# Optimization experiments

Measured on AMD Instinct MI355X. Metric: run time of the kernel, lower is better.

## Reference

```python
import jax, jax.numpy as jnp
import numpy as np

N_NODES = 100000
N_EDGES = 800000
F_IN, N_HID, N_CLS = 256, 128, 40


def setup_inputs() -> dict:
    key = jax.random.key(0)
    ks = jax.random.split(key, 6)
    features = jax.random.normal(ks[0], (N_NODES, F_IN), dtype=jnp.float32)
    src = jax.random.randint(ks[1], (N_EDGES,), 0, N_NODES, dtype=jnp.int64)
    dst = jax.random.randint(ks[2], (N_EDGES,), 0, N_NODES, dtype=jnp.int64)
    W1 = jax.random.normal(ks[3], (F_IN, N_HID), dtype=jnp.float32) / np.sqrt(F_IN)
    b1 = jnp.zeros((N_HID,), dtype=jnp.float32)
    W2 = jax.random.normal(ks[4], (N_HID, N_CLS), dtype=jnp.float32) / np.sqrt(N_HID)
    b2 = jnp.zeros((N_CLS,), dtype=jnp.float32)
    return {"features": features, "src": src, "dst": dst,
            "W1": W1, "b1": b1, "W2": W2, "b2": b2}


def reference(features, src, dst, W1, b1, W2, b2):
    # DGL GraphConv with norm='both': h = D_dst^{-1/2} A (D_src^{-1/2} x) W + b
    # Eval mode: dropout(p=0.85) is identity.
    N = features.shape[0]
    ones = jnp.ones(src.shape[0], dtype=features.dtype)
    out_deg = jax.ops.segment_sum(ones, src, num_segments=N)
    in_deg = jax.ops.segment_sum(ones, dst, num_segments=N)
    norm_src = jnp.where(out_deg > 0, out_deg ** -0.5, 0.0)[:, None]  # [N,1]
    norm_dst = jnp.where(in_deg > 0, in_deg ** -0.5, 0.0)[:, None]

    def gconv(x, W, b):
        # project first (in_feats >= out_feats here) to shrink SpMM width
        h = (x * norm_src) @ W                                # [N, out]
        agg = jax.ops.segment_sum(h[src], dst, num_segments=N)  # sparse aggregate
        return agg * norm_dst + b

    x = jax.nn.relu(gconv(features, W1, b1))
    return gconv(x, W2, b2)
```

## Files before the change

### kernel.cpp

```cpp
#include <hip/hip_runtime.h>
#include <hip/hip_bf16.h>
#include <math.h>


#define F_IN  256
#define F_HID 128
#define F_CLS 40

#define RSZ 8192
#define NSL 32

typedef __bf16 bf16_t;
typedef bf16_t bf16x8 __attribute__((ext_vector_type(8)));
typedef float floatx4 __attribute__((ext_vector_type(4)));

static __device__ __forceinline__ unsigned short f2b(float f) {
    __hip_bfloat16 h = __float2bfloat16(f);
    return __builtin_bit_cast(unsigned short, h);
}
static __device__ __forceinline__ float b2f(unsigned short u) {
    return __uint_as_float((unsigned)u << 16);
}
static __device__ __forceinline__ unsigned short f2h(float f) {
    return __builtin_bit_cast(unsigned short, (_Float16)f);
}
static __device__ __forceinline__ float h2f(unsigned short u) {
    return (float)__builtin_bit_cast(_Float16, u);
}

__global__ __launch_bounds__(256) void hist_kernel(
    const int* __restrict__ src, const int* __restrict__ dst,
    unsigned* __restrict__ partial_s, unsigned* __restrict__ partial_d, int E)
{
    __shared__ unsigned h[RSZ];
    const int t = threadIdx.x;
    const int r  = blockIdx.x / NSL;
    const int sl = blockIdx.x % NSL;
    const int lo = r * RSZ;
    const int* __restrict__ keys = blockIdx.y ? dst : src;
    unsigned* __restrict__ part = blockIdx.y ? partial_d : partial_s;

    for (int i = t; i < RSZ; i += 256) h[i] = 0;
    __syncthreads();

    const int slice = (E + NSL - 1) / NSL;
    const int e0 = sl * slice;
    const int e1 = min(E, e0 + slice);

    int e = e0 + t;
    for (; e + 7 * 256 < e1; e += 8 * 256) {
        int k[8];
        #pragma unroll
        for (int i = 0; i < 8; ++i) k[i] = keys[e + i * 256];
        #pragma unroll
        for (int i = 0; i < 8; ++i) {
            unsigned kk = (unsigned)(k[i] - lo);
            if (kk < RSZ) atomicAdd(&h[kk], 1u);
        }
    }
    for (; e < e1; e += 256) {
        unsigned kk = (unsigned)(keys[e] - lo);
        if (kk < RSZ) atomicAdd(&h[kk], 1u);
    }
    __syncthreads();

    unsigned* dst_p = part + (size_t)blockIdx.x * RSZ;
    for (int i = t; i < RSZ; i += 256) dst_p[i] = h[i];
}

__global__ __launch_bounds__(256) void degnorm_kernel(
    const unsigned* __restrict__ partial_s, const unsigned* __restrict__ partial_d,
    int* __restrict__ cnt_dst, float* __restrict__ norm_src,
    float* __restrict__ norm_dst, int N)
{
    int i = blockIdx.x * 256 + threadIdx.x;
    if (i >= N) return;
    int r = i / RSZ;
    int off = i & (RSZ - 1);
    const unsigned* ps = partial_s + (size_t)r * NSL * RSZ + off;
    const unsigned* pd = partial_d + (size_t)r * NSL * RSZ + off;
    unsigned ss = 0, sd = 0;
    #pragma unroll
    for (int sl = 0; sl < NSL; ++sl) {
        ss += ps[(size_t)sl * RSZ];
        sd += pd[(size_t)sl * RSZ];
    }
    cnt_dst[i] = (int)sd;
    norm_src[i] = ss ? 1.0f / sqrtf((float)ss) : 0.0f;
    norm_dst[i] = sd ? 1.0f / sqrtf((float)sd) : 0.0f;
}

__global__ __launch_bounds__(256) void scan1_kernel(const int* __restrict__ cnt,
                                                    int* __restrict__ row_off,
                                                    int* __restrict__ blk_sums, int N) {
    __shared__ int s[256];
    const int t = threadIdx.x;
    const int base = blockIdx.x * 1024 + t * 4;
    int v0 = (base + 0 < N) ? cnt[base + 0] : 0;
    int v1 = (base + 1 < N) ? cnt[base + 1] : 0;
    int v2 = (base + 2 < N) ? cnt[base + 2] : 0;
    int v3 = (base + 3 < N) ? cnt[base + 3] : 0;
    int local = v0 + v1 + v2 + v3;
    s[t] = local;
    __syncthreads();
    for (int off = 1; off < 256; off <<= 1) {
        int x = (t >= off) ? s[t - off] : 0;
        __syncthreads();
        s[t] += x;
        __syncthreads();
    }
    int excl = s[t] - local;
    if (t == 255) blk_sums[blockIdx.x] = s[t];
    if (base + 0 < N) row_off[base + 0] = excl;
    if (base + 1 < N) row_off[base + 1] = excl + v0;
    if (base + 2 < N) row_off[base + 2] = excl + v0 + v1;
    if (base + 3 < N) row_off[base + 3] = excl + v0 + v1 + v2;
}

__global__ __launch_bounds__(256) void scan2_kernel(int* __restrict__ blk_sums, int B) {
    __shared__ int s[256];
    const int t = threadIdx.x;
    int local = (t < B) ? blk_sums[t] : 0;
    s[t] = local;
    __syncthreads();
    for (int off = 1; off < 256; off <<= 1) {
        int x = (t >= off) ? s[t - off] : 0;
        __syncthreads();
        s[t] += x;
        __syncthreads();
    }
    if (t < B) blk_sums[t] = s[t] - local;
}

__global__ __launch_bounds__(256) void scan3_kernel(int* __restrict__ row_off,
                                                    const int* __restrict__ blk_sums,
                                                    int N, int E) {
    const int t = threadIdx.x;
    const int base = blockIdx.x * 1024 + t * 4;
    const int add = blk_sums[blockIdx.x];
    #pragma unroll
    for (int i = 0; i < 4; ++i) {
        int idx = base + i;
        if (idx < N) row_off[idx] += add;
    }
    if (blockIdx.x == 0 && t == 0) row_off[N] = E;
}

__global__ __launch_bounds__(256) void slicepref_kernel(
    unsigned* __restrict__ partial_d, const int* __restrict__ row_off,
    int N, int NRtot)
{
    int idx = blockIdx.x * 256 + threadIdx.x;
    if (idx >= NRtot) return;
    int r = idx / RSZ;
    int i = idx & (RSZ - 1);
    unsigned run = (idx < N) ? (unsigned)row_off[idx] : 0u;
    unsigned* p = partial_d + (size_t)r * NSL * RSZ + i;
    #pragma unroll
    for (int sl = 0; sl < NSL; ++sl) {
        unsigned c = p[(size_t)sl * RSZ];
        p[(size_t)sl * RSZ] = run;
        run += c;
    }
}

__global__ __launch_bounds__(256) void scatter2_kernel(
    const int* __restrict__ src, const int* __restrict__ dst,
    const unsigned* __restrict__ pref, int* __restrict__ csr_src, int E)
{
    __shared__ unsigned cur[RSZ];
    const int t = threadIdx.x;
    const int r  = blockIdx.x / NSL;
    const int sl = blockIdx.x % NSL;
    const int lo = r * RSZ;
    const unsigned* p = pref + (size_t)blockIdx.x * RSZ;

    for (int i = t; i < RSZ; i += 256) cur[i] = p[i];
    __syncthreads();

    const int slice = (E + NSL - 1) / NSL;
    const int e0 = sl * slice;
    const int e1 = min(E, e0 + slice);

    int e = e0 + t;
    for (; e + 7 * 256 < e1; e += 8 * 256) {
        int d[8], s[8];
        #pragma unroll
        for (int i = 0; i < 8; ++i) { d[i] = dst[e + i * 256]; s[i] = src[e + i * 256]; }
        #pragma unroll
        for (int i = 0; i < 8; ++i) {
            unsigned k = (unsigned)(d[i] - lo);
            if (k < RSZ) {
                unsigned pos = atomicAdd(&cur[k], 1u);
                csr_src[pos] = s[i];
            }
        }
    }
    for (; e < e1; e += 256) {
        unsigned k = (unsigned)(dst[e] - lo);
        if (k < RSZ) {
            unsigned pos = atomicAdd(&cur[k], 1u);
            csr_src[pos] = src[e];
        }
    }
}

__global__ __launch_bounds__(256) void pack_w1t_kernel(const float* __restrict__ W1,
                                                       __hip_bfloat16* __restrict__ W1t) {
    int idx = blockIdx.x * 256 + threadIdx.x;
    int n = idx >> 8;
    int k = idx & 255;
    W1t[idx] = __float2bfloat16(W1[(size_t)k * F_HID + n]);
}

__global__ __launch_bounds__(512, 4) void gemm1_mfma_kernel(
    const float* __restrict__ X, const __hip_bfloat16* __restrict__ W1t,
    const float* __restrict__ norm_src, __hip_bfloat16* __restrict__ h1b, int N)
{
    __shared__ __hip_bfloat16 Bs[128 * 256];
    const int t = threadIdx.x;
    const int node0 = blockIdx.x * 128;
    const int lane = t & 63;
    const int w = t >> 6;
    const int l15 = lane & 15;
    const int quad = lane >> 4;

    const int arow = node0 + w * 16 + l15;
    const bool valid = arow < N;
    const int arow_c = valid ? arow : (N - 1);
    const float ns = valid ? norm_src[arow] : 0.0f;

    const float* xp = X + (size_t)arow_c * F_IN + quad * 8;

    float4 araw[4];
    araw[0] = *(const float4*)(xp + 0);
    araw[1] = *(const float4*)(xp + 4);
    araw[2] = *(const float4*)(xp + 32);
    araw[3] = *(const float4*)(xp + 36);

    #pragma unroll
    for (int i = 0; i < 8; ++i) {
        int idx = i * 512 + t;
        int row = idx >> 5;
        int ch  = idx & 31;
        uint4 v = *(const uint4*)(W1t + (size_t)row * F_IN + ch * 8);
        int d = row * 256 + ((ch * 8) ^ ((row & 7) << 3));
        *(uint4*)(Bs + d) = v;
    }
    __syncthreads();

    const int swz = (l15 & 7) << 3;
    const int bbase0 = l15 * 256 + ((quad * 8) ^ swz);
    const int bbase1 = l15 * 256 + ((32 + quad * 8) ^ swz);

    floatx4 acc[8] = {};

    #pragma unroll
    for (int c = 0; c < 4; ++c) {
        bf16x8 ab0, ab1;
        {
            union { bf16x8 v; unsigned short u[8]; } cv;
            cv.u[0] = f2b(araw[0].x * ns); cv.u[1] = f2b(araw[0].y * ns);
            cv.u[2] = f2b(araw[0].z * ns); cv.u[3] = f2b(araw[0].w * ns);
            cv.u[4] = f2b(araw[1].x * ns); cv.u[5] = f2b(araw[1].y * ns);
            cv.u[6] = f2b(araw[1].z * ns); cv.u[7] = f2b(araw[1].w * ns);
            ab0 = cv.v;
            cv.u[0] = f2b(araw[2].x * ns); cv.u[1] = f2b(araw[2].y * ns);
            cv.u[2] = f2b(araw[2].z * ns); cv.u[3] = f2b(araw[2].w * ns);
            cv.u[4] = f2b(araw[3].x * ns); cv.u[5] = f2b(araw[3].y * ns);
            cv.u[6] = f2b(araw[3].z * ns); cv.u[7] = f2b(araw[3].w * ns);
            ab1 = cv.v;
        }
        if (c < 3) {
            araw[0] = *(const float4*)(xp + (c + 1) * 64 + 0);
            araw[1] = *(const float4*)(xp + (c + 1) * 64 + 4);
            araw[2] = *(const float4*)(xp + (c + 1) * 64 + 32);
            araw[3] = *(const float4*)(xp + (c + 1) * 64 + 36);
        }
        #pragma unroll
        for (int nt = 0; nt < 8; ++nt) {
            bf16x8 b = *(const bf16x8*)(Bs + bbase0 + nt * 16 * 256 + c * 64);
            acc[nt] = __builtin_amdgcn_mfma_f32_16x16x32_bf16(ab0, b, acc[nt], 0, 0, 0);
        }
        #pragma unroll
        for (int nt = 0; nt < 8; ++nt) {
            bf16x8 b = *(const bf16x8*)(Bs + bbase1 + nt * 16 * 256 + c * 64);
            acc[nt] = __builtin_amdgcn_mfma_f32_16x16x32_bf16(ab1, b, acc[nt], 0, 0, 0);
        }
    }

    #pragma unroll
    for (int nt = 0; nt < 8; ++nt) {
        #pragma unroll
        for (int r = 0; r < 4; ++r) {
            int node = node0 + w * 16 + quad * 4 + r;
            if (node < N)
                h1b[(size_t)node * F_HID + nt * 16 + l15] = __float2bfloat16(acc[nt][r]);
        }
    }
}

__global__ __launch_bounds__(256) void spmm1_csr_kernel(
    const __hip_bfloat16* __restrict__ h1b, const int* __restrict__ row_off,
    const int* __restrict__ csr_src, const float* __restrict__ norm_src,
    const float* __restrict__ norm_dst, const float* __restrict__ b1,
    unsigned short* __restrict__ h1act, int N)
{
    const int t = threadIdx.x;
    const int node = blockIdx.x * 8 + (t >> 5);
    if (node >= N) return;
    const int c = (t & 31) << 2;
    const int start = row_off[node];
    const int end = row_off[node + 1];
    float4 acc = make_float4(0.f, 0.f, 0.f, 0.f);
    int j = start;
    for (; j + 8 <= end; j += 8) {
        int s[8];
        #pragma unroll
        for (int i = 0; i < 8; ++i) s[i] = csr_src[j + i];
        ushort4 u[8];
        #pragma unroll
        for (int i = 0; i < 8; ++i)
            u[i] = *(const ushort4*)(h1b + (size_t)s[i] * F_HID + c);
        #pragma unroll
        for (int i = 0; i < 8; ++i) {
            acc.x += b2f(u[i].x);
            acc.y += b2f(u[i].y);
            acc.z += b2f(u[i].z);
            acc.w += b2f(u[i].w);
        }
    }
    for (; j + 2 <= end; j += 2) {
        int s0 = csr_src[j + 0];
        int s1 = csr_src[j + 1];
        ushort4 u0 = *(const ushort4*)(h1b + (size_t)s0 * F_HID + c);
        ushort4 u1 = *(const ushort4*)(h1b + (size_t)s1 * F_HID + c);
        acc.x += b2f(u0.x) + b2f(u1.x);
        acc.y += b2f(u0.y) + b2f(u1.y);
        acc.z += b2f(u0.z) + b2f(u1.z);
        acc.w += b2f(u0.w) + b2f(u1.w);
    }
    if (j < end) {
        int s = csr_src[j];
        ushort4 u = *(const ushort4*)(h1b + (size_t)s * F_HID + c);
        acc.x += b2f(u.x);
        acc.y += b2f(u.y);
        acc.z += b2f(u.z);
        acc.w += b2f(u.w);
    }
    const float nd = norm_dst[node];
    const float ns = norm_src[node];
    float4 bb = *(const float4*)(b1 + c);
    ushort4 o;
    o.x = f2h(fmaxf(fmaf(acc.x, nd, bb.x), 0.f) * ns);
    o.y = f2h(fmaxf(fmaf(acc.y, nd, bb.y), 0.f) * ns);
    o.z = f2h(fmaxf(fmaf(acc.z, nd, bb.z), 0.f) * ns);
    o.w = f2h(fmaxf(fmaf(acc.w, nd, bb.w), 0.f) * ns);
    *(ushort4*)(h1act + (size_t)node * F_HID + c) = o;
}

__global__ __launch_bounds__(320) void gemm2_kernel(
    const unsigned short* __restrict__ h1act, const float* __restrict__ W2,
    unsigned short* __restrict__ h2, int N)
{
    __shared__ float As[64][132];
    __shared__ float Ws[128][40];
    const int t = threadIdx.x;
    const int node0 = blockIdx.x * 64;

    #pragma unroll
    for (int i = 0; i < 4; ++i) {
        int f = t + 320 * i;
        int r = f / 10;
        int kk = (f % 10) * 4;
        *(float4*)&Ws[r][kk] = *(const float4*)(W2 + (size_t)r * F_CLS + kk);
    }
    for (int f = t; f < 2048; f += 320) {
        int r = f >> 5;
        int kk = (f & 31) << 2;
        int node = node0 + r;
        float4 v = make_float4(0.f, 0.f, 0.f, 0.f);
        if (node < N) {
            ushort4 u = *(const ushort4*)(h1act + (size_t)node * F_HID + kk);
            v.x = h2f(u.x); v.y = h2f(u.y); v.z = h2f(u.z); v.w = h2f(u.w);
        }
        *(float4*)&As[r][kk] = v;
    }
    __syncthreads();

    const int col = t % 40;
    const int rowg = t / 40;
    float acc[8] = {};
    #pragma unroll 8
    for (int k = 0; k < F_HID; ++k) {
        float w = Ws[k][col];
        #pragma unroll
        for (int i = 0; i < 8; ++i)
            acc[i] = fmaf(As[rowg * 8 + i][k], w, acc[i]);
    }
    #pragma unroll
    for (int i = 0; i < 8; ++i) {
        int node = node0 + rowg * 8 + i;
        if (node < N) h2[(size_t)node * F_CLS + col] = f2h(acc[i]);
    }
}

__global__ __launch_bounds__(256) void spmm2_csr_kernel(
    const unsigned short* __restrict__ h2, const int* __restrict__ row_off,
    const int* __restrict__ csr_src, const float* __restrict__ norm_dst,
    const float* __restrict__ b2, float* __restrict__ out, int N)
{
    const int t = threadIdx.x;
    const int node = blockIdx.x * 16 + (t >> 4);
    const int lane = t & 15;
    if (node >= N || lane >= 10) return;
    const int c = lane << 2;
    const int start = row_off[node];
    const int end = row_off[node + 1];
    float4 acc = make_float4(0.f, 0.f, 0.f, 0.f);
    int j = start;
    for (; j + 8 <= end; j += 8) {
        int s[8];
        #pragma unroll
        for (int i = 0; i < 8; ++i) s[i] = csr_src[j + i];
        ushort4 u[8];
        #pragma unroll
        for (int i = 0; i < 8; ++i)
            u[i] = *(const ushort4*)(h2 + (size_t)s[i] * F_CLS + c);
        #pragma unroll
        for (int i = 0; i < 8; ++i) {
            acc.x += h2f(u[i].x);
            acc.y += h2f(u[i].y);
            acc.z += h2f(u[i].z);
            acc.w += h2f(u[i].w);
        }
    }
    for (; j + 2 <= end; j += 2) {
        int s0 = csr_src[j + 0];
        int s1 = csr_src[j + 1];
        ushort4 u0 = *(const ushort4*)(h2 + (size_t)s0 * F_CLS + c);
        ushort4 u1 = *(const ushort4*)(h2 + (size_t)s1 * F_CLS + c);
        acc.x += h2f(u0.x) + h2f(u1.x);
        acc.y += h2f(u0.y) + h2f(u1.y);
        acc.z += h2f(u0.z) + h2f(u1.z);
        acc.w += h2f(u0.w) + h2f(u1.w);
    }
    if (j < end) {
        int s = csr_src[j];
        ushort4 u = *(const ushort4*)(h2 + (size_t)s * F_CLS + c);
        acc.x += h2f(u.x);
        acc.y += h2f(u.y);
        acc.z += h2f(u.z);
        acc.w += h2f(u.w);
    }
    float nd = norm_dst[node];
    float4 bb = *(const float4*)(b2 + c);
    float4 r;
    r.x = fmaf(acc.x, nd, bb.x);
    r.y = fmaf(acc.y, nd, bb.y);
    r.z = fmaf(acc.z, nd, bb.z);
    r.w = fmaf(acc.w, nd, bb.w);
    *(float4*)(out + (size_t)node * F_CLS + c) = r;
}

extern "C" void kernel_launch(void* const* d_in, const int* in_sizes, int n_in,
                              void* d_out, int out_size, void* d_ws, size_t ws_size,
                              hipStream_t stream) {
    const float* X   = (const float*)d_in[0];
    const int*   src = (const int*)d_in[1];
    const int*   dst = (const int*)d_in[2];
    const float* W1  = (const float*)d_in[3];
    const float* b1  = (const float*)d_in[4];
    const float* W2  = (const float*)d_in[5];
    const float* b2  = (const float*)d_in[6];
    float* out = (float*)d_out;

    const int N = in_sizes[0] / F_IN;
    const int E = in_sizes[1];
    const int NB = (N + 1023) / 1024;
    const int NR = (N + RSZ - 1) / RSZ;
    const int NRtot = NR * RSZ;

    char* w = (char*)d_ws;
    int*   cnt_dst  = (int*)w;                      w += (size_t)N * 4;
    int*   row_off  = (int*)w;                      w += (size_t)(N + 4) * 4;
    int*   blk_sums = (int*)w;                      w += 256 * 4;
    int*   csr_src  = (int*)w;                      w += (size_t)E * 4;
    float* norm_src = (float*)w;                    w += (size_t)N * 4;
    float* norm_dst = (float*)w;                    w += (size_t)N * 4;
    unsigned short* h1act = (unsigned short*)w;     w += (size_t)N * F_HID * 2;
    unsigned short* h2    = (unsigned short*)w;     w += (size_t)N * F_CLS * 2;
    __hip_bfloat16* W1t = (__hip_bfloat16*)w;       w += (size_t)F_HID * F_IN * 2;
    __hip_bfloat16* h1b = (__hip_bfloat16*)w;       w += (size_t)N * F_HID * 2;
    unsigned* partial_s = (unsigned*)w;             w += (size_t)NR * NSL * RSZ * 4;
    unsigned* partial_d = (unsigned*)w;             w += (size_t)NR * NSL * RSZ * 4;

    hist_kernel<<<dim3(NR * NSL, 2), 256, 0, stream>>>(src, dst, partial_s, partial_d, E);
    degnorm_kernel<<<(N + 255) / 256, 256, 0, stream>>>(partial_s, partial_d,
                                                        cnt_dst, norm_src, norm_dst, N);

    scan1_kernel<<<NB, 256, 0, stream>>>(cnt_dst, row_off, blk_sums, N);
    scan2_kernel<<<1, 256, 0, stream>>>(blk_sums, NB);
    scan3_kernel<<<NB, 256, 0, stream>>>(row_off, blk_sums, N, E);

    slicepref_kernel<<<(NRtot + 255) / 256, 256, 0, stream>>>(partial_d, row_off, N, NRtot);
    scatter2_kernel<<<NR * NSL, 256, 0, stream>>>(src, dst, partial_d, csr_src, E);

    pack_w1t_kernel<<<(F_HID * F_IN) / 256, 256, 0, stream>>>(W1, W1t);

    gemm1_mfma_kernel<<<(N + 127) / 128, 512, 0, stream>>>(X, W1t, norm_src, h1b, N);

    spmm1_csr_kernel<<<(N + 7) / 8, 256, 0, stream>>>(h1b, row_off, csr_src,
                                                      norm_src, norm_dst, b1, h1act, N);

    gemm2_kernel<<<(N + 63) / 64, 320, 0, stream>>>(h1act, W2, h2, N);

    spmm2_csr_kernel<<<(N + 15) / 16, 256, 0, stream>>>(h2, row_off, csr_src, norm_dst, b2, out, N);
}
```

Measured before the change: 347.8 us.

## Replace sliced LDS histogram CSR build with global atomic counting and scatter

Replaces the range-partitioned shared-memory histogram, per-slice prefix and sliced scatter with direct global atomics: one kernel counts source and destination degrees, and one scatter kernel claims CSR positions through atomic cursors. Degree normalisation moves into the first scan kernel, and the W1 transpose is folded into the zeroing prep kernel, so fewer launches remain. The large partial-count buffers and their repeated passes over the edge lists go away. In exchange the build relies on contended global atomics, and the order of edges within each row is no longer deterministic.

```diff
diff --git a/kernel.cpp b/kernel.cpp
--- a/kernel.cpp
+++ b/kernel.cpp
@@ -7,9 +7,6 @@
 #define F_HID 128
 #define F_CLS 40
 
-#define RSZ 8192
-#define NSL 32
-
 typedef __bf16 bf16_t;
 typedef bf16_t bf16x8 __attribute__((ext_vector_type(8)));
 typedef float floatx4 __attribute__((ext_vector_type(4)));
@@ -28,71 +25,47 @@
     return (float)__builtin_bit_cast(_Float16, u);
 }
 
-__global__ __launch_bounds__(256) void hist_kernel(
+__global__ __launch_bounds__(256) void prep_kernel(
+    const float* __restrict__ W1, __hip_bfloat16* __restrict__ W1t,
+    int* __restrict__ cnt_src, int* __restrict__ cnt_dst, int N)
+{
+    int idx = blockIdx.x * 256 + threadIdx.x;
+    if (idx < F_HID * F_IN) {
+        int n = idx >> 8;
+        int k = idx & 255;
+        W1t[idx] = __float2bfloat16(W1[(size_t)k * F_HID + n]);
+    }
+    if (idx < N) {
+        cnt_src[idx] = 0;
+        cnt_dst[idx] = 0;
+    }
+}
+
+__global__ __launch_bounds__(256) void deg_kernel(
     const int* __restrict__ src, const int* __restrict__ dst,
-    unsigned* __restrict__ partial_s, unsigned* __restrict__ partial_d, int E)
-{
-    __shared__ unsigned h[RSZ];
-    const int t = threadIdx.x;
-    const int r  = blockIdx.x / NSL;
-    const int sl = blockIdx.x % NSL;
-    const int lo = r * RSZ;
-    const int* __restrict__ keys = blockIdx.y ? dst : src;
-    unsigned* __restrict__ part = blockIdx.y ? partial_d : partial_s;
-
-    for (int i = t; i < RSZ; i += 256) h[i] = 0;
-    __syncthreads();
-
-    const int slice = (E + NSL - 1) / NSL;
-    const int e0 = sl * slice;
-    const int e1 = min(E, e0 + slice);
-
-    int e = e0 + t;
-    for (; e + 7 * 256 < e1; e += 8 * 256) {
-        int k[8];
-        #pragma unroll
-        for (int i = 0; i < 8; ++i) k[i] = keys[e + i * 256];
-        #pragma unroll
-        for (int i = 0; i < 8; ++i) {
-            unsigned kk = (unsigned)(k[i] - lo);
-            if (kk < RSZ) atomicAdd(&h[kk], 1u);
-        }
-    }
-    for (; e < e1; e += 256) {
-        unsigned kk = (unsigned)(keys[e] - lo);
-        if (kk < RSZ) atomicAdd(&h[kk], 1u);
-    }
-    __syncthreads();
-
-    unsigned* dst_p = part + (size_t)blockIdx.x * RSZ;
-    for (int i = t; i < RSZ; i += 256) dst_p[i] = h[i];
-}
-
-__global__ __launch_bounds__(256) void degnorm_kernel(
-    const unsigned* __restrict__ partial_s, const unsigned* __restrict__ partial_d,
-    int* __restrict__ cnt_dst, float* __restrict__ norm_src,
-    float* __restrict__ norm_dst, int N)
-{
-    int i = blockIdx.x * 256 + threadIdx.x;
-    if (i >= N) return;
-    int r = i / RSZ;
-    int off = i & (RSZ - 1);
-    const unsigned* ps = partial_s + (size_t)r * NSL * RSZ + off;
-    const unsigned* pd = partial_d + (size_t)r * NSL * RSZ + off;
-    unsigned ss = 0, sd = 0;
-    #pragma unroll
-    for (int sl = 0; sl < NSL; ++sl) {
-        ss += ps[(size_t)sl * RSZ];
-        sd += pd[(size_t)sl * RSZ];
-    }
-    cnt_dst[i] = (int)sd;
-    norm_src[i] = ss ? 1.0f / sqrtf((float)ss) : 0.0f;
-    norm_dst[i] = sd ? 1.0f / sqrtf((float)sd) : 0.0f;
-}
-
-__global__ __launch_bounds__(256) void scan1_kernel(const int* __restrict__ cnt,
-                                                    int* __restrict__ row_off,
-                                                    int* __restrict__ blk_sums, int N) {
+    int* __restrict__ cnt_src, int* __restrict__ cnt_dst, int E)
+{
+    int e = (blockIdx.x * 256 + threadIdx.x) * 4;
+    if (e + 4 <= E) {
+        int4 s = *(const int4*)(src + e);
+        int4 d = *(const int4*)(dst + e);
+        atomicAdd(&cnt_src[s.x], 1); atomicAdd(&cnt_src[s.y], 1);
+        atomicAdd(&cnt_src[s.z], 1); atomicAdd(&cnt_src[s.w], 1);
+        atomicAdd(&cnt_dst[d.x], 1); atomicAdd(&cnt_dst[d.y], 1);
+        atomicAdd(&cnt_dst[d.z], 1); atomicAdd(&cnt_dst[d.w], 1);
+    } else {
+        for (int k = e; k < E; ++k) {
+            atomicAdd(&cnt_src[src[k]], 1);
+            atomicAdd(&cnt_dst[dst[k]], 1);
+        }
+    }
+}
+
+__global__ __launch_bounds__(256) void scan1_kernel(
+    const int* __restrict__ cnt, const int* __restrict__ cnt_s,
+    int* __restrict__ row_off, int* __restrict__ blk_sums,
+    float* __restrict__ norm_src, float* __restrict__ norm_dst, int N)
+{
     __shared__ int s[256];
     const int t = threadIdx.x;
     const int base = blockIdx.x * 1024 + t * 4;
@@ -100,6 +73,28 @@
     int v1 = (base + 1 < N) ? cnt[base + 1] : 0;
     int v2 = (base + 2 < N) ? cnt[base + 2] : 0;
     int v3 = (base + 3 < N) ? cnt[base + 3] : 0;
+
+    if (base + 0 < N) {
+        int s0 = cnt_s[base + 0];
+        norm_dst[base + 0] = v0 ? 1.0f / sqrtf((float)v0) : 0.0f;
+        norm_src[base + 0] = s0 ? 1.0f / sqrtf((float)s0) : 0.0f;
+    }
+    if (base + 1 < N) {
+        int s1 = cnt_s[base + 1];
+        norm_dst[base + 1] = v1 ? 1.0f / sqrtf((float)v1) : 0.0f;
+        norm_src[base + 1] = s1 ? 1.0f / sqrtf((float)s1) : 0.0f;
+    }
+    if (base + 2 < N) {
+        int s2 = cnt_s[base + 2];
+        norm_dst[base + 2] = v2 ? 1.0f / sqrtf((float)v2) : 0.0f;
+        norm_src[base + 2] = s2 ? 1.0f / sqrtf((float)s2) : 0.0f;
+    }
+    if (base + 3 < N) {
+        int s3 = cnt_s[base + 3];
+        norm_dst[base + 3] = v3 ? 1.0f / sqrtf((float)v3) : 0.0f;
+        norm_src[base + 3] = s3 ? 1.0f / sqrtf((float)s3) : 0.0f;
+    }
+
     int local = v0 + v1 + v2 + v3;
     s[t] = local;
     __syncthreads();
@@ -132,85 +127,47 @@
     if (t < B) blk_sums[t] = s[t] - local;
 }
 
-__global__ __launch_bounds__(256) void scan3_kernel(int* __restrict__ row_off,
-                                                    const int* __restrict__ blk_sums,
-                                                    int N, int E) {
+__global__ __launch_bounds__(256) void scan3_kernel(
+    int* __restrict__ row_off, const int* __restrict__ blk_sums,
+    int* __restrict__ cur, int N, int E)
+{
     const int t = threadIdx.x;
     const int base = blockIdx.x * 1024 + t * 4;
     const int add = blk_sums[blockIdx.x];
     #pragma unroll
     for (int i = 0; i < 4; ++i) {
         int idx = base + i;
-        if (idx < N) row_off[idx] += add;
+        if (idx < N) {
+            int v = row_off[idx] + add;
+            row_off[idx] = v;
+            cur[idx] = v;
+        }
     }
     if (blockIdx.x == 0 && t == 0) row_off[N] = E;
 }
 
-__global__ __launch_bounds__(256) void slicepref_kernel(
-    unsigned* __restrict__ partial_d, const int* __restrict__ row_off,
-    int N, int NRtot)
-{
-    int idx = blockIdx.x * 256 + threadIdx.x;
-    if (idx >= NRtot) return;
-    int r = idx / RSZ;
-    int i = idx & (RSZ - 1);
-    unsigned run = (idx < N) ? (unsigned)row_off[idx] : 0u;
-    unsigned* p = partial_d + (size_t)r * NSL * RSZ + i;
-    #pragma unroll
-    for (int sl = 0; sl < NSL; ++sl) {
-        unsigned c = p[(size_t)sl * RSZ];
-        p[(size_t)sl * RSZ] = run;
-        run += c;
-    }
-}
-
-__global__ __launch_bounds__(256) void scatter2_kernel(
+__global__ __launch_bounds__(256) void scatter_atomic_kernel(
     const int* __restrict__ src, const int* __restrict__ dst,
-    const unsigned* __restrict__ pref, int* __restrict__ csr_src, int E)
-{
-    __shared__ unsigned cur[RSZ];
-    const int t = threadIdx.x;
-    const int r  = blockIdx.x / NSL;
-    const int sl = blockIdx.x % NSL;
-    const int lo = r * RSZ;
-    const unsigned* p = pref + (size_t)blockIdx.x * RSZ;
-
-    for (int i = t; i < RSZ; i += 256) cur[i] = p[i];
-    __syncthreads();
-
-    const int slice = (E + NSL - 1) / NSL;
-    const int e0 = sl * slice;
-    const int e1 = min(E, e0 + slice);
-
-    int e = e0 + t;
-    for (; e + 7 * 256 < e1; e += 8 * 256) {
-        int d[8], s[8];
-        #pragma unroll
-        for (int i = 0; i < 8; ++i) { d[i] = dst[e + i * 256]; s[i] = src[e + i * 256]; }
-        #pragma unroll
-        for (int i = 0; i < 8; ++i) {
-            unsigned k = (unsigned)(d[i] - lo);
-            if (k < RSZ) {
-                unsigned pos = atomicAdd(&cur[k], 1u);
-                csr_src[pos] = s[i];
-            }
-        }
-    }
-    for (; e < e1; e += 256) {
-        unsigned k = (unsigned)(dst[e] - lo);
-        if (k < RSZ) {
-            unsigned pos = atomicAdd(&cur[k], 1u);
-            csr_src[pos] = src[e];
-        }
-    }
-}
-
-__global__ __launch_bounds__(256) void pack_w1t_kernel(const float* __restrict__ W1,
-                                                       __hip_bfloat16* __restrict__ W1t) {
-    int idx = blockIdx.x * 256 + threadIdx.x;
-    int n = idx >> 8;
-    int k = idx & 255;
-    W1t[idx] = __float2bfloat16(W1[(size_t)k * F_HID + n]);
+    int* __restrict__ cur, int* __restrict__ csr_src, int E)
+{
+    int e = (blockIdx.x * 256 + threadIdx.x) * 4;
+    if (e + 4 <= E) {
+        int4 s = *(const int4*)(src + e);
+        int4 d = *(const int4*)(dst + e);
+        int p0 = atomicAdd(&cur[d.x], 1);
+        int p1 = atomicAdd(&cur[d.y], 1);
+        int p2 = atomicAdd(&cur[d.z], 1);
+        int p3 = atomicAdd(&cur[d.w], 1);
+        csr_src[p0] = s.x;
+        csr_src[p1] = s.y;
+        csr_src[p2] = s.z;
+        csr_src[p3] = s.w;
+    } else {
+        for (int k = e; k < E; ++k) {
+            int p = atomicAdd(&cur[dst[k]], 1);
+            csr_src[p] = src[k];
+        }
+    }
 }
 
 __global__ __launch_bounds__(512, 4) void gemm1_mfma_kernel(
@@ -478,11 +435,11 @@
     const int N = in_sizes[0] / F_IN;
     const int E = in_sizes[1];
     const int NB = (N + 1023) / 1024;
-    const int NR = (N + RSZ - 1) / RSZ;
-    const int NRtot = NR * RSZ;
 
     char* w = (char*)d_ws;
+    int*   cnt_src  = (int*)w;                      w += (size_t)N * 4;
     int*   cnt_dst  = (int*)w;                      w += (size_t)N * 4;
+    int*   cur      = (int*)w;                      w += (size_t)N * 4;
     int*   row_off  = (int*)w;                      w += (size_t)(N + 4) * 4;
     int*   blk_sums = (int*)w;                      w += 256 * 4;
     int*   csr_src  = (int*)w;                      w += (size_t)E * 4;
@@ -492,21 +449,18 @@
     unsigned short* h2    = (unsigned short*)w;     w += (size_t)N * F_CLS * 2;
     __hip_bfloat16* W1t = (__hip_bfloat16*)w;       w += (size_t)F_HID * F_IN * 2;
     __hip_bfloat16* h1b = (__hip_bfloat16*)w;       w += (size_t)N * F_HID * 2;
-    unsigned* partial_s = (unsigned*)w;             w += (size_t)NR * NSL * RSZ * 4;
-    unsigned* partial_d = (unsigned*)w;             w += (size_t)NR * NSL * RSZ * 4;
-
-    hist_kernel<<<dim3(NR * NSL, 2), 256, 0, stream>>>(src, dst, partial_s, partial_d, E);
-    degnorm_kernel<<<(N + 255) / 256, 256, 0, stream>>>(partial_s, partial_d,
-                                                        cnt_dst, norm_src, norm_dst, N);
-
-    scan1_kernel<<<NB, 256, 0, stream>>>(cnt_dst, row_off, blk_sums, N);
+
+    const int prep_n = (N > F_HID * F_IN) ? N : F_HID * F_IN;
+    prep_kernel<<<(prep_n + 255) / 256, 256, 0, stream>>>(W1, W1t, cnt_src, cnt_dst, N);
+
+    deg_kernel<<<(E / 4 + 255) / 256, 256, 0, stream>>>(src, dst, cnt_src, cnt_dst, E);
+
+    scan1_kernel<<<NB, 256, 0, stream>>>(cnt_dst, cnt_src, row_off, blk_sums,
+                                         norm_src, norm_dst, N);
     scan2_kernel<<<1, 256, 0, stream>>>(blk_sums, NB);
-    scan3_kernel<<<NB, 256, 0, stream>>>(row_off, blk_sums, N, E);
-
-    slicepref_kernel<<<(NRtot + 255) / 256, 256, 0, stream>>>(partial_d, row_off, N, NRtot);
-    scatter2_kernel<<<NR * NSL, 256, 0, stream>>>(src, dst, partial_d, csr_src, E);
-
-    pack_w1t_kernel<<<(F_HID * F_IN) / 256, 256, 0, stream>>>(W1, W1t);
+    scan3_kernel<<<NB, 256, 0, stream>>>(row_off, blk_sums, cur, N, E);
+
+    scatter_atomic_kernel<<<(E / 4 + 255) / 256, 256, 0, stream>>>(src, dst, cur, csr_src, E);
 
     gemm1_mfma_kernel<<<(N + 127) / 128, 512, 0, stream>>>(X, W1t, norm_src, h1b, N);
 
```

After: 403.6 us. 1.16x slower.
